# Kernel tuning notes

Hardware: AMD Instinct MI355X
Metric: run time of the kernel (lower is better)

## Reference

```python
import jax, jax.numpy as jnp
import numpy as np

# ---- module constants (from init_kwargs) ----
GRID = np.array([160, 160, 160], dtype=np.int32)
CENTER = np.array([0.0, 0.0, 0.0], dtype=np.float32)
SIZE = np.array([200.0, 200.0, 200.0], dtype=np.float32)
KERNEL_WIDTH = 3.0
N_SAMPLES = 128   # line-integral samples per LOR (ray-driven TOR approximation)
N_LORS = 50000

_CORNERS = [(dx, dy, dz) for dx in (0, 1) for dy in (0, 1) for dz in (0, 1)]


def _sample_line(lors, grid, center, size, n_samples, dtype):
    """lors: [N,6] (p1 xyz, p2 xyz). Returns base voxel idx i0 [N,S,3],
    trilinear fracs w [N,S,3], per-sample step length [N]."""
    p1, p2 = lors[:, 0:3], lors[:, 3:6]
    t = (jnp.arange(n_samples, dtype=dtype) + 0.5) / n_samples          # [S]
    pos = p1[:, None, :] + t[None, :, None] * (p2 - p1)[:, None, :]     # [N,S,3]
    step = jnp.linalg.norm(p2 - p1, axis=-1) / n_samples                # [N]
    gridf = grid.astype(np.float32)
    vsize = size / gridf
    origin = center - 0.5 * size
    f = (pos - origin) / vsize - 0.5        # continuous voxel-center coords
    f = jnp.clip(f, 0.0, gridf - 1.0)
    i0 = jnp.clip(jnp.floor(f).astype(jnp.int32), 0, grid - 2)          # [N,S,3]
    w = f - i0.astype(dtype)                                            # [N,S,3]
    return i0, w, step


def _corner_weight(w, c):
    dx, dy, dz = c
    wx = w[..., 0] if dx else 1.0 - w[..., 0]
    wy = w[..., 1] if dy else 1.0 - w[..., 1]
    wz = w[..., 2] if dz else 1.0 - w[..., 2]
    return wx * wy * wz


def projection(lors, image, grid, center, size, kernel_width):
    """Ray-driven line integrals through image. lors [N,6] -> [N]."""
    i0, w, step = _sample_line(lors, grid, center, size, N_SAMPLES, image.dtype)
    val = jnp.zeros(i0.shape[:2], image.dtype)   # [N,S]
    for c in _CORNERS:
        dx, dy, dz = c
        val = val + _corner_weight(w, c) * image[i0[..., 0] + dx,
                                                 i0[..., 1] + dy,
                                                 i0[..., 2] + dz]
    return kernel_width * step * val.sum(axis=1)  # [N]


def backprojection(image, grid, lors, center, size, line_integral, kernel_width):
    """Scatter line_integral back along the same rays -> volume like image."""
    i0, w, step = _sample_line(lors, grid, center, size, N_SAMPLES, image.dtype)
    contrib = (kernel_width * line_integral * step)[:, None]  # [N,1] -> bcast [N,S]
    bp = jnp.zeros(image.shape, image.dtype)
    for c in _CORNERS:
        dx, dy, dz = c
        bp = bp.at[i0[..., 0] + dx, i0[..., 1] + dy, i0[..., 2] + dz].add(
            _corner_weight(w, c) * contrib)
    return bp


def _tor_step(image, efficiency_map, xlors, ylors, zlors):
    imgz = image
    imgx = jnp.transpose(imgz, (2, 0, 1))
    imgy = jnp.transpose(imgz, (1, 0, 2))
    xl = jnp.transpose(xlors)  # [N,6]
    yl = jnp.transpose(ylors)
    zl = jnp.transpose(zlors)

    # z-direction (native axis order)
    pz = projection(zl, imgz, GRID, CENTER, SIZE, KERNEL_WIDTH)
    bpz = backprojection(imgz, GRID, zl, CENTER, SIZE, pz, KERNEL_WIDTH)

    # x-direction: permuted frame (y, z, x)
    gx = GRID[[1, 2, 0]]; cx = CENTER[[1, 2, 0]]; sx = SIZE[[1, 2, 0]]
    px = projection(xl, imgx, gx, cx, sx, KERNEL_WIDTH)
    bpx = backprojection(imgx, gx, xl, cx, sx, px, KERNEL_WIDTH)
    bpxt = jnp.transpose(bpx, (1, 2, 0))

    # y-direction: permuted frame (x, z, y)
    gy = GRID[[0, 2, 1]]; cy = CENTER[[0, 2, 1]]; sy = SIZE[[0, 2, 1]]
    py = projection(yl, imgy, gy, cy, sy, KERNEL_WIDTH)
    bpy = backprojection(imgy, gy, yl, cy, sy, py, KERNEL_WIDTH)
    bpyt = jnp.transpose(bpy, (1, 0, 2))

    return imgz * efficiency_map * (bpxt + bpyt + bpz)


def setup_inputs() -> dict:
    key = jax.random.key(0)
    k_img, k_eff, kx, ky, kz = jax.random.split(key, 5)
    image = jax.random.uniform(k_img, tuple(GRID), dtype=jnp.float32)
    effmap = jax.random.uniform(k_eff, tuple(GRID), dtype=jnp.float32)
    lo = jnp.asarray(np.concatenate([CENTER - 0.5 * SIZE] * 2), jnp.float32)   # [6]
    span = jnp.asarray(np.concatenate([SIZE] * 2), jnp.float32)                # [6]
    def mk(k):
        u = jax.random.uniform(k, (6, N_LORS), dtype=jnp.float32)
        return u * span[:, None] + lo[:, None]
    return {"image": image, "efficiency_map": effmap,
            "xlors": mk(kx), "ylors": mk(ky), "zlors": mk(kz)}


def reference(image, efficiency_map, xlors, ylors, zlors):
    return _tor_step(image, efficiency_map, xlors, ylors, zlors)
```

## Files before the change

### kernel.cpp

```cpp
#include <hip/hip_runtime.h>

#define NL 50000
#define NS 128
#define G 160
#define GSQ (160*160)
#define GCUBE (160*160*160)
#define NRB 196
#define NBINS (G*2)
#define ENT_CAP 11500000

struct RayParam { float4 a, b; };

__device__ __forceinline__ void lds_add(float* p, float v) {
    atomicAdd(p, v);
}

__device__ __forceinline__ float frcp(float x) {
#if __has_builtin(__builtin_amdgcn_rcpf)
    return __builtin_amdgcn_rcpf(x);
#else
    return 1.0f / x;
#endif
}

__device__ __forceinline__ void coordf(float pos, int& i, float& w) {
    float f = (pos + 100.0f) * 0.8f - 0.5f;
    f = fminf(fmaxf(f, 0.0f), 159.0f);
    int ii = (int)f; ii = ii > 158 ? 158 : ii;
    i = ii; w = f - (float)ii;
}

__device__ __forceinline__ int cnt_for(float A, float B, float rB, int p, int& slo_out) {
    const float glo = (p <= 1)   ? -1.0f  : (float)(p - 1);
    const float ghi = (p >= 158) ? 160.0f : (float)(p + 1);
    int slo, shi;
    if (B == 0.0f) {
        if (A < glo || A > ghi) { slo_out = 0; return 0; }
        slo = 0; shi = NS - 1;
    } else {
        const float t1 = (glo - A) * rB, t2 = (ghi - A) * rB;
        const float tlo = fminf(t1, t2), thi = fmaxf(t1, t2);
        float slof = ceilf (tlo * (float)NS - 0.75f);
        float shif = floorf(thi * (float)NS - 0.25f);
        slof = fminf(fmaxf(slof,  0.0f), 127.0f);
        shif = fminf(fmaxf(shif, -1.0f), 127.0f);
        slo = (int)slof; shi = (int)shif;
    }
    slo_out = slo;
    return shi - slo + 1;
}

__device__ __forceinline__ void halves_for(
    float A, float B, float rB, int p, float AR, float BR,
    int& lo0, int& n0, int& lo1, int& n1)
{
    lo0 = lo1 = 0; n0 = n1 = 0;
    int slo; const int c = cnt_for(A, B, rB, p, slo);
    if (c <= 0) return;
    const int shi = slo + c - 1;
    if (BR == 0.0f) {
        if (AR < 80.0f) { lo0 = slo; n0 = c; } else { lo1 = slo; n1 = c; }
        return;
    }
    float sstar = ((80.0f - AR) * frcp(BR)) * (float)NS - 0.5f;
    sstar = fminf(fmaxf(sstar, -300.0f), 300.0f);
    float lo0f, hi0f, lo1f, hi1f;
    if (BR > 0.0f) {
        lo0f = (float)slo;  hi0f = fminf((float)shi, floorf(sstar) + 1.0f);
        lo1f = fmaxf((float)slo, ceilf(sstar) - 1.0f);  hi1f = (float)shi;
    } else {
        lo1f = (float)slo;  hi1f = fminf((float)shi, floorf(sstar) + 1.0f);
        lo0f = fmaxf((float)slo, ceilf(sstar) - 1.0f);  hi0f = (float)shi;
    }
    lo0 = (int)lo0f; n0 = (int)hi0f - lo0 + 1; if (n0 < 0) n0 = 0;
    lo1 = (int)lo1f; n1 = (int)hi1f - lo1 + 1; if (n1 < 0) n1 = 0;
}

__device__ __forceinline__ void plane_range(float A, float B, int& plo, int& phi) {
    const float f0 = A + B * (0.5f / NS);
    const float f1 = A + B * (((float)NS - 0.5f) / NS);
    const float fmn = fminf(f0, f1), fmx = fmaxf(f0, f1);
    plo = (int)fmaxf(ceilf (fmn - 1.01f), 0.0f);
    phi = (int)fminf(floorf(fmx + 1.01f), 159.0f);
}

template<int PA, int PB, int PC, int QS, int QR, int QC>
__device__ __forceinline__ void proj_body(
    const float* __restrict__ img,
    const float* __restrict__ lors,
    float* __restrict__ contrib,
    RayParam* __restrict__ params,
    int sa, int sb, int bx)
{
    const int wave = threadIdx.x >> 6;
    const int lane = threadIdx.x & 63;
    const int lor  = bx * 4 + wave;

    const float p1x = lors[0*NL + lor];
    const float p1y = lors[1*NL + lor];
    const float p1z = lors[2*NL + lor];
    const float dxv = lors[3*NL + lor] - p1x;
    const float dyv = lors[4*NL + lor] - p1y;
    const float dzv = lors[5*NL + lor] - p1z;
    const float len  = sqrtf(dxv*dxv + dyv*dyv + dzv*dzv);
    const float step = len * (1.0f/NS);

    float sum = 0.0f;
    #pragma unroll
    for (int q = 0; q < 2; ++q) {
        const int s = lane + q*64;
        const float t = ((float)s + 0.5f) * (1.0f/NS);
        const float pos[3] = { p1x + t*dxv, p1y + t*dyv, p1z + t*dzv };
        int ia, ib, ic; float wa, wb, wc;
        coordf(pos[PA], ia, wa);
        coordf(pos[PB], ib, wb);
        coordf(pos[PC], ic, wc);
        const float* g = img + ia*sa + ib*sb + ic;
        const float v000 = g[0],       v001 = g[1];
        const float v010 = g[sb],      v011 = g[sb + 1];
        const float v100 = g[sa],      v101 = g[sa + 1];
        const float v110 = g[sa + sb], v111 = g[sa + sb + 1];
        const float c00 = v000 + wc*(v001 - v000);
        const float c01 = v010 + wc*(v011 - v010);
        const float c10 = v100 + wc*(v101 - v100);
        const float c11 = v110 + wc*(v111 - v110);
        const float c0  = c00 + wb*(c01 - c00);
        const float c1  = c10 + wb*(c11 - c10);
        sum += c0 + wa*(c1 - c0);
    }

    #pragma unroll
    for (int off = 32; off > 0; off >>= 1)
        sum += __shfl_xor(sum, off, 64);

    if (lane == 0) {
        const float cb = 9.0f * step * step * sum;
        contrib[lor] = cb;
        if (params) {
            const float P1v[3] = { p1x, p1y, p1z };
            const float DVv[3] = { dxv, dyv, dzv };
            float4 a, b;
            a.x = (P1v[QS] + 100.0f)*0.8f - 0.5f;  a.y = DVv[QS]*0.8f;
            a.z = (P1v[QR] + 100.0f)*0.8f - 0.5f;  a.w = DVv[QR]*0.8f;
            b.x = (P1v[QC] + 100.0f)*0.8f - 0.5f;  b.y = DVv[QC]*0.8f;
            b.z = cb;                               b.w = 0.0f;
            params[lor].a = a;
            params[lor].b = b;
        }
    }
}

__global__ __launch_bounds__(256) void proj_all(
    const float* __restrict__ img,
    const float* __restrict__ xl, const float* __restrict__ yl,
    const float* __restrict__ zl,
    float* __restrict__ cz, float* __restrict__ cx, float* __restrict__ cy,
    RayParam* __restrict__ params)
{
    const int bx = blockIdx.x;
    if (blockIdx.y == 0)
        proj_body<0,1,2, 0,1,2>(img, zl, cz, params ? params        : nullptr, GSQ, G, bx);
    else if (blockIdx.y == 1)
        proj_body<1,2,0, 1,2,0>(img, xl, cx, params ? params +   NL : nullptr, GSQ, G, bx);
    else
        proj_body<0,1,2, 1,0,2>(img, yl, cy, params ? params + 2*NL : nullptr, G, GSQ, bx);
}

__global__ __launch_bounds__(256) void bin_count(
    const RayParam* __restrict__ params, int* __restrict__ totals)
{
    const int rb = blockIdx.x, pass = blockIdx.y;
    __shared__ int cnt[NBINS];
    for (int i = threadIdx.x; i < NBINS; i += 256) cnt[i] = 0;
    __syncthreads();

    const int r = rb*256 + threadIdx.x;
    if (r < NL) {
        const float4 a = params[pass*NL + r].a;
        const float A = a.x, B = a.y, AR = a.z, BR = a.w;
        int plo, phi; plane_range(A, B, plo, phi);
        const float rB = frcp(B);
        for (int p = plo; p <= phi; ++p) {
            int lo0, n0, lo1, n1;
            halves_for(A, B, rB, p, AR, BR, lo0, n0, lo1, n1);
            if (n0 > 0) atomicAdd(&cnt[p*2    ], (n0 + 7) >> 3);
            if (n1 > 0) atomicAdd(&cnt[p*2 + 1], (n1 + 7) >> 3);
        }
    }
    __syncthreads();
    for (int i = threadIdx.x; i < NBINS; i += 256)
        if (cnt[i]) atomicAdd(&totals[i], cnt[i]);
}

__global__ __launch_bounds__(512) void scan320(
    const int* __restrict__ totals, int* __restrict__ offsets,
    int* __restrict__ cur)
{
    __shared__ int v[NBINS];
    const int tid = threadIdx.x;
    int mine = 0;
    if (tid < NBINS) { mine = totals[tid]; v[tid] = mine; }
    __syncthreads();
    for (int off = 1; off < NBINS; off <<= 1) {
        int x = 0;
        if (tid < NBINS && tid >= off) x = v[tid - off];
        __syncthreads();
        if (tid < NBINS) v[tid] += x;
        __syncthreads();
    }
    if (tid < NBINS) {
        const int excl = v[tid] - mine;
        offsets[tid] = excl;
        cur[tid]     = excl;
    }
    if (tid == 0) offsets[NBINS] = v[NBINS-1];
}

__global__ __launch_bounds__(256) void bin_write(
    const RayParam* __restrict__ params, int* __restrict__ cur,
    unsigned* __restrict__ entries)
{
    const int rb = blockIdx.x, pass = blockIdx.y;
    __shared__ int cnt[NBINS];
    __shared__ int base[NBINS];
    for (int i = threadIdx.x; i < NBINS; i += 256) cnt[i] = 0;
    __syncthreads();

    const int r = rb*256 + threadIdx.x;
    float A = 0, B = 0, AR = 0, BR = 0, rB = 0;
    int plo = 0, phi = -1;
    if (r < NL) {
        const float4 a = params[pass*NL + r].a;
        A = a.x; B = a.y; AR = a.z; BR = a.w;
        plane_range(A, B, plo, phi);
        rB = frcp(B);
        for (int p = plo; p <= phi; ++p) {
            int lo0, n0, lo1, n1;
            halves_for(A, B, rB, p, AR, BR, lo0, n0, lo1, n1);
            if (n0 > 0) atomicAdd(&cnt[p*2    ], (n0 + 7) >> 3);
            if (n1 > 0) atomicAdd(&cnt[p*2 + 1], (n1 + 7) >> 3);
        }
    }
    __syncthreads();
    for (int i = threadIdx.x; i < NBINS; i += 256) {
        const int c = cnt[i];
        base[i] = c ? atomicAdd(&cur[i], c) : 0;
    }
    __syncthreads();
    for (int i = threadIdx.x; i < NBINS; i += 256) cnt[i] = 0;
    __syncthreads();

    if (r < NL) {
        for (int p = plo; p <= phi; ++p) {
            int lo0, n0, lo1, n1;
            halves_for(A, B, rB, p, AR, BR, lo0, n0, lo1, n1);
            #pragma unroll
            for (int h = 0; h < 2; ++h) {
                const int lo = h ? lo1 : lo0;
                const int n  = h ? n1  : n0;
                if (n > 0) {
                    const int bin = p*2 + h;
                    const int ke = (n + 7) >> 3;
                    const int gb = base[bin] + atomicAdd(&cnt[bin], ke);
                    for (int e = 0; e < ke; ++e) {
                        const int s0 = lo + e*8;
                        const int nn = (n - e*8) < 8 ? (n - e*8) : 8;
                        const unsigned enc = (unsigned)r | ((unsigned)s0 << 17)
                                           | ((unsigned)(nn-1) << 24)
                                           | ((unsigned)pass << 27);
                        if (gb + e < ENT_CAP) entries[gb + e] = enc;
                    }
                }
            }
        }
    }
}

__global__ __launch_bounds__(512) void bp_half(
    const RayParam* __restrict__ params, const int* __restrict__ offsets,
    const unsigned* __restrict__ entries,
    float* __restrict__ out)
{
    __shared__ float tile[81*G];
    const int b   = blockIdx.x;
    const int c   = blockIdx.y;
    const int p   = b >> 1;
    const int h   = b & 1;
    const int tid = threadIdx.x;
    const int rowbase = 80 * h;

    for (int j = tid; j < 81*G; j += 512) tile[j] = 0.0f;
    __syncthreads();

    int s0 = offsets[b];
    int e0 = offsets[b+1];
    if (e0 > ENT_CAP) e0 = ENT_CAP;
    if (s0 > e0) s0 = e0;
    const int n  = e0 - s0;
    const int cs = s0 + (n *  c     ) / 2;
    const int ce = s0 + (n * (c + 1)) / 2;

    int e = cs + tid;
    unsigned enc = 0; RayParam rp;
    if (e < ce) {
        enc = entries[e];
        rp  = params[(enc >> 27)*NL + (enc & 0x1FFFF)];
    }

    int   pk  = -1;
    float a00 = 0.0f, a01 = 0.0f, a10 = 0.0f, a11 = 0.0f;

    while (e < ce) {
        const int en = e + 512;
        unsigned encN = 0;
        if (en < ce) encN = entries[en];

        const int ss = (enc >> 17) & 0x7F;
        const int nn = ((enc >> 24) & 0x7) + 1;
        const float A = rp.a.x, B = rp.a.y, AR = rp.a.z, BR = rp.a.w;
        const float AC = rp.b.x, BC = rp.b.y, cb = rp.b.z;

        for (int i = 0; i < nn; ++i) {
            const float t = ((float)(ss + i) + 0.5f) * (1.0f/NS);
            float fA = A + B*t;
            fA = fminf(fmaxf(fA, 0.0f), 159.0f);
            int ia = (int)fA; ia = ia > 158 ? 158 : ia;
            const float wa = fA - (float)ia;
            float fa;
            if (ia == p)          fa = 1.0f - wa;
            else if (ia == p - 1) fa = wa;
            else                  fa = -1.0f;

            float fR = AR + BR*t;
            fR = fminf(fmaxf(fR, 0.0f), 159.0f);
            int ib = (int)fR; ib = ib > 158 ? 158 : ib;
            const int rl = ib - rowbase;

            if (fa >= 0.0f && rl >= 0 && rl <= 79) {
                float fC = AC + BC*t;
                fC = fminf(fmaxf(fC, 0.0f), 159.0f);
                int ic = (int)fC; ic = ic > 158 ? 158 : ic;
                const float wb = fR - (float)ib;
                const float wc = fC - (float)ic;
                const float v  = fa * cb;
                const float v0 = v * (1.0f - wb), v1 = v * wb;
                const int key = rl*G + ic;
                if (key != pk) {
                    if (pk >= 0) {
                        float* q = tile + pk;
                        lds_add(q,         a00);
                        lds_add(q + 1,     a01);
                        lds_add(q + G,     a10);
                        lds_add(q + G + 1, a11);
                    }
                    pk = key;
                    a00 = 0.0f; a01 = 0.0f; a10 = 0.0f; a11 = 0.0f;
                }
                a00 += v0 * (1.0f - wc);
                a01 += v0 * wc;
                a10 += v1 * (1.0f - wc);
                a11 += v1 * wc;
            }
        }

        if (en < ce)
            rp = params[(encN >> 27)*NL + (encN & 0x1FFFF)];
        enc = encN; e = en;
    }

    if (pk >= 0) {
        float* q = tile + pk;
        lds_add(q,         a00);
        lds_add(q + 1,     a01);
        lds_add(q + G,     a10);
        lds_add(q + G + 1, a11);
    }
    __syncthreads();

    const int nrows = h ? 80 : 81;
    float* dst = out + (size_t)p * GSQ + (size_t)rowbase * G;
    for (int j = tid; j < nrows*G; j += 512) {
#if __has_builtin(__builtin_amdgcn_global_atomic_fadd_f32)
        unsafeAtomicAdd(&dst[j], tile[j]);
#else
        atomicAdd(&dst[j], tile[j]);
#endif
    }
}

__global__ __launch_bounds__(256) void finalize_mul(
    const float4* __restrict__ img, const float4* __restrict__ eff,
    float4* __restrict__ out)
{
    const int i = blockIdx.x * 256 + threadIdx.x;
    const float4 a = img[i];
    const float4 e = eff[i];
    float4 o = out[i];
    o.x *= a.x * e.x;
    o.y *= a.y * e.y;
    o.z *= a.z * e.z;
    o.w *= a.w * e.w;
    out[i] = o;
}

template<int PS, int PR, int PC2>
__device__ __forceinline__ void slab_accum(
    float* __restrict__ plane,
    const float* __restrict__ lors,
    const float* __restrict__ contrib,
    int p, int wave, int lane, int nwaves)
{
    for (int base = wave*64; base < NL; base += nwaves*64) {
        const int r = base + lane;
        float A = 0.f, B = 0.f, AR = 0.f, BR = 0.f, AC = 0.f, BC = 0.f, cb = 0.f;
        int slo = 0, cnt = 0;
        if (r < NL) {
            const float q0 = lors[0*NL + r], q1 = lors[1*NL + r], q2 = lors[2*NL + r];
            const float d0 = lors[3*NL + r] - q0;
            const float d1 = lors[4*NL + r] - q1;
            const float d2 = lors[5*NL + r] - q2;
            const float P1[3] = { q0, q1, q2 };
            const float DV[3] = { d0, d1, d2 };
            A  = (P1[PS]  + 100.0f)*0.8f - 0.5f;  B  = DV[PS]*0.8f;
            AR = (P1[PR]  + 100.0f)*0.8f - 0.5f;  BR = DV[PR]*0.8f;
            AC = (P1[PC2] + 100.0f)*0.8f - 0.5f;  BC = DV[PC2]*0.8f;
            cb = contrib[r];
            const float rB = frcp(B);
            cnt = cnt_for(A, B, rB, p, slo);
            if (cnt < 0) cnt = 0;
        }

        int pref = cnt;
        #pragma unroll
        for (int off = 1; off < 64; off <<= 1) {
            const int nsh = __shfl_up(pref, off, 64);
            if (lane >= off) pref += nsh;
        }
        const int total = __shfl(pref, 63, 64);
        const int start = pref - cnt;

        for (int k0 = 0; k0 < total; k0 += 64) {
            const int k  = k0 + lane;
            const int kc = k < total ? k : total - 1;

            int j = 0;
            #pragma unroll
            for (int stp = 32; stp >= 1; stp >>= 1) {
                const int cand = j + stp;
                const int sc = __shfl(start, cand, 64);
                if (cand < 64 && sc <= kc) j = cand;
            }

            const int   sj  = __shfl(slo,   j, 64);
            const int   stj = __shfl(start, j, 64);
            const float Aj  = __shfl(A,  j, 64);
            const float Bj  = __shfl(B,  j, 64);
            const float ARj = __shfl(AR, j, 64);
            const float BRj = __shfl(BR, j, 64);
            const float ACj = __shfl(AC, j, 64);
            const float BCj = __shfl(BC, j, 64);
            const float cbj = __shfl(cb, j, 64);

            const int s = sj + (kc - stj);
            const float t = ((float)s + 0.5f) * (1.0f/NS);
            float fA = Aj + Bj * t;
            fA = fminf(fmaxf(fA, 0.0f), 159.0f);
            int ia = (int)fA; ia = ia > 158 ? 158 : ia;
            const float wa = fA - (float)ia;
            float fa;
            if (ia == p)          fa = 1.0f - wa;
            else if (ia == p - 1) fa = wa;
            else                  fa = -1.0f;

            float fR = ARj + BRj * t;
            float fC = ACj + BCj * t;
            fR = fminf(fmaxf(fR, 0.0f), 159.0f);
            fC = fminf(fmaxf(fC, 0.0f), 159.0f);
            int ib = (int)fR; ib = ib > 158 ? 158 : ib;
            int ic = (int)fC; ic = ic > 158 ? 158 : ic;
            const float wb = fR - (float)ib;
            const float wc = fC - (float)ic;

            if (k < total && fa >= 0.0f) {
                const float v  = fa * cbj;
                const float v0 = v * (1.0f - wb), v1 = v * wb;
                float* q = plane + ib*G + ic;
                lds_add(q,         v0 * (1.0f - wc));
                lds_add(q + 1,     v0 * wc);
                lds_add(q + G,     v1 * (1.0f - wc));
                lds_add(q + G + 1, v1 * wc);
            }
        }
    }
}

__global__ __launch_bounds__(1024) void bp_fused(
    const float* __restrict__ img, const float* __restrict__ eff,
    const float* __restrict__ zl, const float* __restrict__ xl,
    const float* __restrict__ yl,
    const float* __restrict__ cz, const float* __restrict__ cx,
    const float* __restrict__ cy,
    float* __restrict__ out)
{
    __shared__ float plane[GSQ];
    const int p    = blockIdx.x;
    const int tid  = threadIdx.x;
    const int wave = tid >> 6;
    const int lane = tid & 63;

    for (int j = tid; j < GSQ; j += 1024) plane[j] = 0.0f;
    __syncthreads();

    slab_accum<0,1,2>(plane, zl, cz, p, wave, lane, 16);
    slab_accum<1,2,0>(plane, xl, cx, p, wave, lane, 16);
    slab_accum<1,0,2>(plane, yl, cy, p, wave, lane, 16);

    __syncthreads();

    const int pbase = p * GSQ;
    for (int j = tid; j < GSQ; j += 1024) {
        const int idx = pbase + j;
        out[idx] = plane[j] * img[idx] * eff[idx];
    }
}

extern "C" void kernel_launch(void* const* d_in, const int* in_sizes, int n_in,
                              void* d_out, int out_size, void* d_ws, size_t ws_size,
                              hipStream_t stream) {
    const float* img = (const float*)d_in[0];
    const float* eff = (const float*)d_in[1];
    const float* xl  = (const float*)d_in[2];
    const float* yl  = (const float*)d_in[3];
    const float* zl  = (const float*)d_in[4];
    float* out = (float*)d_out;

    const size_t CONTRIB_B = (size_t)3*NL*sizeof(float);
    const size_t PARAMS_B  = (size_t)3*NL*sizeof(RayParam);
    const size_t TOT_B     = (size_t)NBINS*sizeof(int);
    const size_t OFFS_B    = (size_t)(NBINS+1)*sizeof(int);
    const size_t CUR_B     = (size_t)NBINS*sizeof(int);
    const size_t ENT_B     = (size_t)ENT_CAP*sizeof(unsigned);

    char* w = (char*)d_ws;
    float*    cz      = (float*)w;
    float*    cx      = cz + NL;
    float*    cy      = cx + NL;
    RayParam* params  = (RayParam*)(w + CONTRIB_B);
    int*      totals  = (int*)(w + CONTRIB_B + PARAMS_B);
    int*      offsets = (int*)(w + CONTRIB_B + PARAMS_B + TOT_B);
    int*      cur     = (int*)(w + CONTRIB_B + PARAMS_B + TOT_B + OFFS_B);
    unsigned* entries = (unsigned*)(w + CONTRIB_B + PARAMS_B + TOT_B + OFFS_B + CUR_B);

    const bool binned =
        ws_size >= CONTRIB_B + PARAMS_B + TOT_B + OFFS_B + CUR_B + ENT_B;

    proj_all<<<dim3(NL/4, 3), dim3(256), 0, stream>>>(
        img, xl, yl, zl, cz, cx, cy, binned ? params : nullptr);

    if (binned) {
        hipMemsetAsync(out, 0, (size_t)GCUBE * sizeof(float), stream);
        hipMemsetAsync(totals, 0, TOT_B, stream);
        bin_count<<<dim3(NRB, 3), dim3(256), 0, stream>>>(params, totals);
        scan320  <<<dim3(1),      dim3(512), 0, stream>>>(totals, offsets, cur);
        bin_write<<<dim3(NRB, 3), dim3(256), 0, stream>>>(params, cur, entries);
        bp_half  <<<dim3(NBINS,2),dim3(512), 0, stream>>>(params, offsets, entries, out);
        finalize_mul<<<dim3(GCUBE/4/256), dim3(256), 0, stream>>>(
            (const float4*)img, (const float4*)eff, (float4*)out);
    } else {
        bp_fused<<<dim3(G), dim3(1024), 0, stream>>>(
            img, eff, zl, xl, yl, cz, cx, cy, out);
    }
}
```

Before: 1.255 ms.

## Assign contiguous entry ranges per thread and vectorize projection gathers

In the backprojection scatter kernel, each thread now walks a contiguous slice of the entry list instead of striding by the block size. Consecutive entries from the same ray can then reuse the loaded ray parameters and keep merging into the register accumulator, which cuts parameter reloads and LDS atomic flushes. The projection kernel now fetches each pair of z-adjacent voxels with a single 8-byte load and issues all loads before the interpolation arithmetic to raise memory-level parallelism. Risks include uneven work per thread, uncoalesced entry reads, and misaligned 8-byte loads when the base index is odd.

Result: slower. 1.389 ms (+10.6%).

```diff
diff --git a/kernel.cpp b/kernel.cpp
--- a/kernel.cpp
+++ b/kernel.cpp
@@ -105,7 +105,9 @@
     const float len  = sqrtf(dxv*dxv + dyv*dyv + dzv*dzv);
     const float step = len * (1.0f/NS);
 
-    float sum = 0.0f;
+    float2 P00[2], P01[2], P10[2], P11[2];
+    float waq[2], wbq[2], wcq[2];
+
     #pragma unroll
     for (int q = 0; q < 2; ++q) {
         const int s = lane + q*64;
@@ -116,14 +118,21 @@
         coordf(pos[PB], ib, wb);
         coordf(pos[PC], ic, wc);
         const float* g = img + ia*sa + ib*sb + ic;
-        const float v000 = g[0],       v001 = g[1];
-        const float v010 = g[sb],      v011 = g[sb + 1];
-        const float v100 = g[sa],      v101 = g[sa + 1];
-        const float v110 = g[sa + sb], v111 = g[sa + sb + 1];
-        const float c00 = v000 + wc*(v001 - v000);
-        const float c01 = v010 + wc*(v011 - v010);
-        const float c10 = v100 + wc*(v101 - v100);
-        const float c11 = v110 + wc*(v111 - v110);
+        __builtin_memcpy(&P00[q], g,            8);
+        __builtin_memcpy(&P01[q], g + sb,       8);
+        __builtin_memcpy(&P10[q], g + sa,       8);
+        __builtin_memcpy(&P11[q], g + sa + sb,  8);
+        waq[q] = wa; wbq[q] = wb; wcq[q] = wc;
+    }
+
+    float sum = 0.0f;
+    #pragma unroll
+    for (int q = 0; q < 2; ++q) {
+        const float wa = waq[q], wb = wbq[q], wc = wcq[q];
+        const float c00 = P00[q].x + wc*(P00[q].y - P00[q].x);
+        const float c01 = P01[q].x + wc*(P01[q].y - P01[q].x);
+        const float c10 = P10[q].x + wc*(P10[q].y - P10[q].x);
+        const float c11 = P11[q].x + wc*(P11[q].y - P11[q].x);
         const float c0  = c00 + wb*(c01 - c00);
         const float c1  = c10 + wb*(c11 - c10);
         sum += c0 + wa*(c1 - c0);
@@ -299,21 +308,23 @@
     const int n  = e0 - s0;
     const int cs = s0 + (n *  c     ) / 2;
     const int ce = s0 + (n * (c + 1)) / 2;
-
-    int e = cs + tid;
-    unsigned enc = 0; RayParam rp;
-    if (e < ce) {
-        enc = entries[e];
-        rp  = params[(enc >> 27)*NL + (enc & 0x1FFFF)];
-    }
+    const int cn = ce - cs;
+
+    const int my_s = cs + (int)(((long long)cn * tid)       >> 9);
+    const int my_e = cs + (int)(((long long)cn * (tid + 1)) >> 9);
 
     int   pk  = -1;
     float a00 = 0.0f, a01 = 0.0f, a10 = 0.0f, a11 = 0.0f;
 
-    while (e < ce) {
-        const int en = e + 512;
+    unsigned enc = 0; RayParam rp;
+    if (my_s < my_e) {
+        enc = entries[my_s];
+        rp  = params[(enc >> 27)*NL + (enc & 0x1FFFF)];
+    }
+
+    for (int e = my_s; e < my_e; ++e) {
         unsigned encN = 0;
-        if (en < ce) encN = entries[en];
+        if (e + 1 < my_e) encN = entries[e + 1];
 
         const int ss = (enc >> 17) & 0x7F;
         const int nn = ((enc >> 24) & 0x7) + 1;
@@ -363,9 +374,11 @@
             }
         }
 
-        if (en < ce)
-            rp = params[(encN >> 27)*NL + (encN & 0x1FFFF)];
-        enc = encN; e = en;
+        if (e + 1 < my_e) {
+            if (((encN ^ enc) & 0x1801FFFFu) != 0u)
+                rp = params[(encN >> 27)*NL + (encN & 0x1FFFF)];
+        }
+        enc = encN;
     }
 
     if (pk >= 0) {
```
